# Kernel tuning notes

Measured on AMD Instinct MI355X. Metric: run time of the kernel, lower is better.

The kernel has to match this reference:

```python
import jax, jax.numpy as jnp
import numpy as np


def setup_inputs() -> dict:
    key = jax.random.key(0)
    ks = jax.random.split(key, 6)
    b, l, d, n = 4, 2048, 1024, 16
    scale_d = 1.0 / np.sqrt(d)
    x = jax.random.normal(ks[0], (b, l, d), dtype=jnp.float32)
    W1 = jax.random.normal(ks[1], (d, d), dtype=jnp.float32) * scale_d
    b1 = jnp.zeros((d,), dtype=jnp.float32)
    W2 = jax.random.normal(ks[2], (n, d), dtype=jnp.float32) * scale_d
    b2 = jnp.zeros((n,), dtype=jnp.float32)
    W3 = jax.random.normal(ks[3], (n, d), dtype=jnp.float32) * scale_d
    b3 = jnp.zeros((n,), dtype=jnp.float32)
    A = jax.random.normal(ks[4], (d, n), dtype=jnp.float32) * np.sqrt(2.0 / (d + n))
    return {"x": x, "W1": W1, "b1": b1, "W2": W2, "b2": b2, "W3": W3, "b3": b3, "A": A}


def reference(x, W1, b1, W2, b2, W3, b3, A):
    # delta = softplus(fc1(x)); B = fc2(x); C = fc3(x)
    delta = jax.nn.softplus(jnp.einsum('bld,ed->ble', x, W1) + b1)   # (b,l,d)
    B = jnp.einsum('bld,nd->bln', x, W2) + b2                         # (b,l,n)
    C = jnp.einsum('bld,nd->bln', x, W3) + b3                         # (b,l,n)
    # Discretization: dB = delta \otimes B; dA = exp(delta \otimes A).
    # In the original forward, h is zero-initialized so dA * h == 0 exactly
    # (for both values and gradients); h_new = x[...,None] * dB.
    dB = jnp.einsum('bld,bln->bldn', delta, B)                        # (b,l,d,n)
    h = x[..., None] * dB                                             # (b,l,d,n)
    y = jnp.einsum('bln,bldn->bld', C, h)                             # (b,l,d)
    return y
```

## Files before the change

### kernel.cpp

```cpp
#include <hip/hip_runtime.h>
#include <hip/hip_bf16.h>

typedef __attribute__((ext_vector_type(8))) short bf16x8;
typedef __attribute__((ext_vector_type(8))) unsigned short u16x8;
typedef __attribute__((ext_vector_type(4))) float f32x4;

#define DDIM 1024
#define BM 256
#define BN 128
#define BK 64

__device__ __forceinline__ void gload_lds16(const void* g, void* l) {
  __builtin_amdgcn_global_load_lds((const __attribute__((address_space(1))) void*)g,
                                   (__attribute__((address_space(3))) void*)l,
                                   16, 0, 0);
}

__device__ __forceinline__ unsigned short f2bf(float f) {
  unsigned int u = __float_as_uint(f);
  unsigned int r = (u + 0x7FFFu + ((u >> 16) & 1u)) >> 16;
  return (unsigned short)r;
}

__global__ __launch_bounds__(256) void s6_convert(
    const float* __restrict__ X, const float* __restrict__ W1,
    const float* __restrict__ W2, const float* __restrict__ W3,
    unsigned short* __restrict__ Xbf, unsigned short* __restrict__ W1bf,
    unsigned short* __restrict__ W2bf, unsigned short* __restrict__ W3bf)
{
  const int wid = threadIdx.x >> 6, lane = threadIdx.x & 63;
  const int row = blockIdx.x * 4 + wid;
  const float* src;
  unsigned short* dst;
  if (row < 8192)      { src = X  + (size_t)row * DDIM;        dst = Xbf  + (size_t)row * DDIM; }
  else if (row < 9216) { int r = row - 8192; src = W1 + (size_t)r * DDIM; dst = W1bf + (size_t)r * DDIM; }
  else if (row < 9232) { int r = row - 9216; src = W2 + (size_t)r * DDIM; dst = W2bf + (size_t)r * DDIM; }
  else                 { int r = row - 9232; src = W3 + (size_t)r * DDIM; dst = W3bf + (size_t)r * DDIM; }

  const float4* s4 = reinterpret_cast<const float4*>(src + lane * 16);
  unsigned short u[16];
  #pragma unroll
  for (int j = 0; j < 4; ++j) {
    float4 v = s4[j];
    u[j*4+0] = f2bf(v.x); u[j*4+1] = f2bf(v.y);
    u[j*4+2] = f2bf(v.z); u[j*4+3] = f2bf(v.w);
  }
  u16x8* d8 = reinterpret_cast<u16x8*>(dst + lane * 16);
  u16x8 lo, hi;
  #pragma unroll
  for (int j = 0; j < 8; ++j) { lo[j] = u[j]; hi[j] = u[j + 8]; }
  d8[0] = lo; d8[1] = hi;
}

__global__ __launch_bounds__(512, 2) void s6_main_fused(
    const unsigned short* __restrict__ Xbf,
    const unsigned short* __restrict__ W1bf,
    const unsigned short* __restrict__ W2bf,
    const unsigned short* __restrict__ W3bf,
    const float* __restrict__ b1,
    const float* __restrict__ b2,
    const float* __restrict__ b3,
    float* __restrict__ Y)
{
  __shared__ __align__(16) unsigned short lds[2 * 16384 + 2 * 12288];
  unsigned short* AB = lds;
  unsigned short* BB = lds + 2 * 16384;

  const int tid  = threadIdx.x;
  const int wid  = tid >> 6;
  const int lane = tid & 63;
  const int tile = (blockIdx.x & 7) * 32 + (blockIdx.x >> 3);
  const int rb   = tile >> 3;
  const int cb   = tile & 7;
  const int row0 = rb * BM;
  const int col0 = cb * BN;
  const int wr = wid >> 1, wc = wid & 1;

  const f32x4 z4 = {0.f, 0.f, 0.f, 0.f};
  f32x4 acc[4][4];
  #pragma unroll
  for (int i = 0; i < 4; ++i)
    #pragma unroll
    for (int j = 0; j < 4; ++j)
      acc[i][j] = z4;
  f32x4 accS[4] = {z4, z4, z4, z4};

  const int srow = tid >> 3;
  const int sdch = (lane & 7) ^ (lane >> 3);
  const unsigned short* gaBase = Xbf  + (size_t)(row0 + srow) * DDIM + sdch * 8;
  const unsigned short* gbBase = W1bf + (size_t)(col0 + srow) * DDIM + sdch * 8;
  const int sub = srow;
  const unsigned short* gwsrc;
  if (sub < 16)      gwsrc = W2bf + (size_t)sub * DDIM;
  else if (sub < 32) gwsrc = W3bf + (size_t)(sub - 16) * DDIM;
  else               gwsrc = W2bf + (size_t)(sub & 15) * DDIM;
  const unsigned short* gwBase = gwsrc + sdch * 8;

  const int fr = lane & 15;
  const int swz0 = (((lane >> 4) + 0) ^ (fr & 7)) * 8;
  const int swz1 = (((lane >> 4) + 4) ^ (fr & 7)) * 8;

#define STAGE(BUF, KEL) do {                                                   \
    const unsigned short* sa_ = gaBase + (KEL);                                \
    const unsigned short* sb_ = gbBase + (KEL);                                \
    unsigned short* la_ = AB + (BUF) * 16384 + wid * 512;                      \
    unsigned short* lb_ = BB + (BUF) * 12288 + wid * 512;                      \
    gload_lds16(sa_,                la_);                                      \
    gload_lds16(sa_ +  64 * DDIM,   la_ + 4096);                               \
    gload_lds16(sa_ + 128 * DDIM,   la_ + 8192);                               \
    gload_lds16(sa_ + 192 * DDIM,   la_ + 12288);                              \
    gload_lds16(sb_,                lb_);                                      \
    gload_lds16(sb_ +  64 * DDIM,   lb_ + 4096);                               \
    gload_lds16(gwBase + (KEL),     lb_ + 8192);                               \
  } while (0)

#define COMPUTE(PAR) do {                                                      \
    const unsigned short* Al = AB + (PAR) * 16384;                             \
    const unsigned short* Bl = BB + (PAR) * 12288;                             \
    bf16x8 af[4][2], bfr[4][2], wfr[2];                                        \
    _Pragma("unroll")                                                          \
    for (int m = 0; m < 4; ++m) {                                              \
      af[m][0] = *reinterpret_cast<const bf16x8*>(&Al[(wr*64 + m*16 + fr)*BK + swz0]); \
      af[m][1] = *reinterpret_cast<const bf16x8*>(&Al[(wr*64 + m*16 + fr)*BK + swz1]); \
    }                                                                          \
    _Pragma("unroll")                                                          \
    for (int n = 0; n < 4; ++n) {                                              \
      bfr[n][0] = *reinterpret_cast<const bf16x8*>(&Bl[(wc*64 + n*16 + fr)*BK + swz0]); \
      bfr[n][1] = *reinterpret_cast<const bf16x8*>(&Bl[(wc*64 + n*16 + fr)*BK + swz1]); \
    }                                                                          \
    wfr[0] = *reinterpret_cast<const bf16x8*>(&Bl[(128 + wc*16 + fr)*BK + swz0]); \
    wfr[1] = *reinterpret_cast<const bf16x8*>(&Bl[(128 + wc*16 + fr)*BK + swz1]); \
    __builtin_amdgcn_s_setprio(1);                                             \
    _Pragma("unroll")                                                          \
    for (int ks = 0; ks < 2; ++ks) {                                           \
      _Pragma("unroll")                                                        \
      for (int m = 0; m < 4; ++m) {                                            \
        _Pragma("unroll")                                                      \
        for (int n = 0; n < 4; ++n)                                            \
          acc[m][n] = __builtin_amdgcn_mfma_f32_16x16x32_bf16(af[m][ks], bfr[n][ks], acc[m][n], 0, 0, 0); \
        accS[m] = __builtin_amdgcn_mfma_f32_16x16x32_bf16(af[m][ks], wfr[ks], accS[m], 0, 0, 0); \
      }                                                                        \
    }                                                                          \
    __builtin_amdgcn_s_setprio(0);                                             \
  } while (0)

#define STEP(J, PAR) do {                                                      \
    if ((J) < 15) {                                                            \
      STAGE((PAR) ^ 1, ((J) + 1) * BK);                                        \
      asm volatile("s_waitcnt vmcnt(7)" ::: "memory");                         \
    } else {                                                                   \
      asm volatile("s_waitcnt vmcnt(0)" ::: "memory");                         \
    }                                                                          \
    __builtin_amdgcn_s_barrier();                                              \
    __builtin_amdgcn_sched_barrier(0);                                         \
    COMPUTE(PAR);                                                              \
    __builtin_amdgcn_s_barrier();                                              \
  } while (0)

  STAGE(0, 0);
  asm volatile("s_waitcnt vmcnt(0)" ::: "memory");
  __builtin_amdgcn_s_barrier();

  for (int jj = 0; jj < 16; jj += 2) {
    STEP(jj, 0);
    STEP(jj + 1, 1);
  }
#undef STEP
#undef COMPUTE
#undef STAGE

  float* sEx = (float*)lds;
  const int n_  = lane & 15;
  const int rgp = (lane >> 4) * 4;
  const float bSelf = (wc == 0 ? b2[n_] : b3[n_]);
  #pragma unroll
  for (int m = 0; m < 4; ++m)
    #pragma unroll
    for (int q = 0; q < 4; ++q)
      sEx[(wc * 256 + wr * 64 + m * 16 + rgp + q) * 17 + n_] = accS[m][q] + bSelf;
  __syncthreads();

  float sv[4][4];
  #pragma unroll
  for (int m = 0; m < 4; ++m) {
    #pragma unroll
    for (int q = 0; q < 4; ++q) {
      const float other = sEx[((wc ^ 1) * 256 + wr * 64 + m * 16 + rgp + q) * 17 + n_];
      float p = (accS[m][q] + bSelf) * other;
      p += __shfl_xor(p, 1, 64);
      p += __shfl_xor(p, 2, 64);
      p += __shfl_xor(p, 4, 64);
      p += __shfl_xor(p, 8, 64);
      sv[m][q] = p;
    }
  }

  #pragma unroll
  for (int m = 0; m < 4; ++m) {
    #pragma unroll
    for (int q = 0; q < 4; ++q) {
      const int gr = row0 + wr * 64 + m * 16 + rgp + q;
      const float svv = sv[m][q];
      const size_t rbase = (size_t)gr * DDIM;
      #pragma unroll
      for (int n = 0; n < 4; ++n) {
        const int gc = col0 + wc * 64 + n * 16 + fr;
        const float z  = acc[m][n][q] + b1[gc];
        const float sp = fmaxf(z, 0.f) + __logf(1.f + __expf(-fabsf(z)));
        const float xv = __bfloat162float(*(const __hip_bfloat16*)&Xbf[rbase + gc]);
        Y[rbase + gc] = xv * svv * sp;
      }
    }
  }
}

extern "C" void kernel_launch(void* const* d_in, const int* in_sizes, int n_in,
                              void* d_out, int out_size, void* d_ws, size_t ws_size,
                              hipStream_t stream) {
  const float* x  = (const float*)d_in[0];
  const float* W1 = (const float*)d_in[1];
  const float* b1 = (const float*)d_in[2];
  const float* W2 = (const float*)d_in[3];
  const float* b2 = (const float*)d_in[4];
  const float* W3 = (const float*)d_in[5];
  const float* b3 = (const float*)d_in[6];

  char* ws = (char*)d_ws;
  unsigned short* Xbf  = (unsigned short*)(ws);
  unsigned short* W1bf = (unsigned short*)(ws + 16777216);
  unsigned short* W2bf = (unsigned short*)(ws + 16777216 + 2097152);
  unsigned short* W3bf = (unsigned short*)(ws + 16777216 + 2097152 + 32768);

  s6_convert<<<2312, 256, 0, stream>>>(x, W1, W2, W3, Xbf, W1bf, W2bf, W3bf);
  s6_main_fused<<<256, 512, 0, stream>>>(Xbf, W1bf, W2bf, W3bf, b1, b2, b3,
                                         (float*)d_out);
}
```

Measured before the change: 44.35 us.

## Interleave global-to-LDS staging with MFMA phases in fine-grained K-loop schedule

Restructures the main GEMM loop into four sub-phases per K-tile. Each phase reads a few LDS fragments, issues part of the next tile's global-to-LDS loads, and runs a group of MFMAs, with barriers and priority hints between phases. The goal is to spread memory issue across compute and lower register pressure by loading fewer fragments at a time. The cost is more barriers and lgkmcnt waits per iteration, which could serialize the waves.

```diff
diff --git a/kernel.cpp b/kernel.cpp
--- a/kernel.cpp
+++ b/kernel.cpp
@@ -100,74 +100,119 @@
   const int swz0 = (((lane >> 4) + 0) ^ (fr & 7)) * 8;
   const int swz1 = (((lane >> 4) + 4) ^ (fr & 7)) * 8;
 
-#define STAGE(BUF, KEL) do {                                                   \
-    const unsigned short* sa_ = gaBase + (KEL);                                \
-    const unsigned short* sb_ = gbBase + (KEL);                                \
-    unsigned short* la_ = AB + (BUF) * 16384 + wid * 512;                      \
-    unsigned short* lb_ = BB + (BUF) * 12288 + wid * 512;                      \
-    gload_lds16(sa_,                la_);                                      \
-    gload_lds16(sa_ +  64 * DDIM,   la_ + 4096);                               \
-    gload_lds16(sa_ + 128 * DDIM,   la_ + 8192);                               \
-    gload_lds16(sa_ + 192 * DDIM,   la_ + 12288);                              \
-    gload_lds16(sb_,                lb_);                                      \
-    gload_lds16(sb_ +  64 * DDIM,   lb_ + 4096);                               \
-    gload_lds16(gwBase + (KEL),     lb_ + 8192);                               \
-  } while (0)
-
-#define COMPUTE(PAR) do {                                                      \
-    const unsigned short* Al = AB + (PAR) * 16384;                             \
-    const unsigned short* Bl = BB + (PAR) * 12288;                             \
-    bf16x8 af[4][2], bfr[4][2], wfr[2];                                        \
-    _Pragma("unroll")                                                          \
-    for (int m = 0; m < 4; ++m) {                                              \
-      af[m][0] = *reinterpret_cast<const bf16x8*>(&Al[(wr*64 + m*16 + fr)*BK + swz0]); \
-      af[m][1] = *reinterpret_cast<const bf16x8*>(&Al[(wr*64 + m*16 + fr)*BK + swz1]); \
-    }                                                                          \
-    _Pragma("unroll")                                                          \
-    for (int n = 0; n < 4; ++n) {                                              \
-      bfr[n][0] = *reinterpret_cast<const bf16x8*>(&Bl[(wc*64 + n*16 + fr)*BK + swz0]); \
-      bfr[n][1] = *reinterpret_cast<const bf16x8*>(&Bl[(wc*64 + n*16 + fr)*BK + swz1]); \
-    }                                                                          \
-    wfr[0] = *reinterpret_cast<const bf16x8*>(&Bl[(128 + wc*16 + fr)*BK + swz0]); \
-    wfr[1] = *reinterpret_cast<const bf16x8*>(&Bl[(128 + wc*16 + fr)*BK + swz1]); \
-    __builtin_amdgcn_s_setprio(1);                                             \
-    _Pragma("unroll")                                                          \
-    for (int ks = 0; ks < 2; ++ks) {                                           \
-      _Pragma("unroll")                                                        \
-      for (int m = 0; m < 4; ++m) {                                            \
-        _Pragma("unroll")                                                      \
-        for (int n = 0; n < 4; ++n)                                            \
-          acc[m][n] = __builtin_amdgcn_mfma_f32_16x16x32_bf16(af[m][ks], bfr[n][ks], acc[m][n], 0, 0, 0); \
-        accS[m] = __builtin_amdgcn_mfma_f32_16x16x32_bf16(af[m][ks], wfr[ks], accS[m], 0, 0, 0); \
-      }                                                                        \
-    }                                                                          \
-    __builtin_amdgcn_s_setprio(0);                                             \
-  } while (0)
-
-#define STEP(J, PAR) do {                                                      \
-    if ((J) < 15) {                                                            \
-      STAGE((PAR) ^ 1, ((J) + 1) * BK);                                        \
-      asm volatile("s_waitcnt vmcnt(7)" ::: "memory");                         \
-    } else {                                                                   \
-      asm volatile("s_waitcnt vmcnt(0)" ::: "memory");                         \
-    }                                                                          \
-    __builtin_amdgcn_s_barrier();                                              \
-    __builtin_amdgcn_sched_barrier(0);                                         \
-    COMPUTE(PAR);                                                              \
-    __builtin_amdgcn_s_barrier();                                              \
-  } while (0)
-
-  STAGE(0, 0);
+#define SA(BUF, KEL, SEG) gload_lds16(gaBase + (KEL) + (SEG) * 64 * DDIM,      \
+                                      AB + (BUF) * 16384 + wid * 512 + (SEG) * 4096)
+#define SB(BUF, KEL, SEG) gload_lds16(gbBase + (KEL) + (SEG) * 64 * DDIM,      \
+                                      BB + (BUF) * 12288 + wid * 512 + (SEG) * 4096)
+#define SW(BUF, KEL)      gload_lds16(gwBase + (KEL),                          \
+                                      BB + (BUF) * 12288 + wid * 512 + 8192)
+#define RA(M, SWZ) (*reinterpret_cast<const bf16x8*>(&Al[(wr * 64 + (M) * 16 + fr) * BK + (SWZ)]))
+#define RB(N, SWZ) (*reinterpret_cast<const bf16x8*>(&Bl[(wc * 64 + (N) * 16 + fr) * BK + (SWZ)]))
+#define RW(SWZ)    (*reinterpret_cast<const bf16x8*>(&Bl[(128 + wc * 16 + fr) * BK + (SWZ)]))
+#define BAR()   __builtin_amdgcn_s_barrier()
+#define SCB()   __builtin_amdgcn_sched_barrier(0)
+#define LGKM0() asm volatile("s_waitcnt lgkmcnt(0)" ::: "memory")
+
+  SA(0, 0, 0); SA(0, 0, 1); SA(0, 0, 2); SA(0, 0, 3);
+  SB(0, 0, 0); SB(0, 0, 1); SW(0, 0);
   asm volatile("s_waitcnt vmcnt(0)" ::: "memory");
-  __builtin_amdgcn_s_barrier();
-
-  for (int jj = 0; jj < 16; jj += 2) {
-    STEP(jj, 0);
-    STEP(jj + 1, 1);
-  }
-#undef STEP
-#undef COMPUTE
-#undef STAGE
+  BAR(); SCB();
+
+  for (int t = 0; t < 16; ++t) {
+    const int par = t & 1;
+    const int nb  = par ^ 1;
+    const int kn  = (t + 1) * BK;
+    const unsigned short* Al = AB + par * 16384;
+    const unsigned short* Bl = BB + par * 12288;
+    bf16x8 a0, a1, a2, a3, f0, f1, f2, f3, wf;
+
+    if (t < 15) {
+      SA(nb, kn, 0); SA(nb, kn, 1);
+      asm volatile("s_waitcnt vmcnt(2)" ::: "memory");
+    } else {
+      asm volatile("s_waitcnt vmcnt(0)" ::: "memory");
+    }
+    BAR(); SCB();
+    a0 = RA(0, swz0); a1 = RA(1, swz0);
+    f0 = RB(0, swz0); f1 = RB(1, swz0); f2 = RB(2, swz0); f3 = RB(3, swz0);
+    wf = RW(swz0);
+    LGKM0(); SCB();
+    __builtin_amdgcn_s_setprio(1);
+    acc[0][0] = __builtin_amdgcn_mfma_f32_16x16x32_bf16(a0, f0, acc[0][0], 0, 0, 0);
+    acc[0][1] = __builtin_amdgcn_mfma_f32_16x16x32_bf16(a0, f1, acc[0][1], 0, 0, 0);
+    acc[0][2] = __builtin_amdgcn_mfma_f32_16x16x32_bf16(a0, f2, acc[0][2], 0, 0, 0);
+    acc[0][3] = __builtin_amdgcn_mfma_f32_16x16x32_bf16(a0, f3, acc[0][3], 0, 0, 0);
+    acc[1][0] = __builtin_amdgcn_mfma_f32_16x16x32_bf16(a1, f0, acc[1][0], 0, 0, 0);
+    acc[1][1] = __builtin_amdgcn_mfma_f32_16x16x32_bf16(a1, f1, acc[1][1], 0, 0, 0);
+    acc[1][2] = __builtin_amdgcn_mfma_f32_16x16x32_bf16(a1, f2, acc[1][2], 0, 0, 0);
+    acc[1][3] = __builtin_amdgcn_mfma_f32_16x16x32_bf16(a1, f3, acc[1][3], 0, 0, 0);
+    __builtin_amdgcn_s_setprio(0);
+    BAR(); SCB();
+
+    a2 = RA(2, swz0); a3 = RA(3, swz0);
+    if (t < 15) { SA(nb, kn, 2); SA(nb, kn, 3); }
+    BAR(); SCB();
+    LGKM0(); SCB();
+    __builtin_amdgcn_s_setprio(1);
+    acc[2][0] = __builtin_amdgcn_mfma_f32_16x16x32_bf16(a2, f0, acc[2][0], 0, 0, 0);
+    acc[2][1] = __builtin_amdgcn_mfma_f32_16x16x32_bf16(a2, f1, acc[2][1], 0, 0, 0);
+    acc[2][2] = __builtin_amdgcn_mfma_f32_16x16x32_bf16(a2, f2, acc[2][2], 0, 0, 0);
+    acc[2][3] = __builtin_amdgcn_mfma_f32_16x16x32_bf16(a2, f3, acc[2][3], 0, 0, 0);
+    acc[3][0] = __builtin_amdgcn_mfma_f32_16x16x32_bf16(a3, f0, acc[3][0], 0, 0, 0);
+    acc[3][1] = __builtin_amdgcn_mfma_f32_16x16x32_bf16(a3, f1, acc[3][1], 0, 0, 0);
+    acc[3][2] = __builtin_amdgcn_mfma_f32_16x16x32_bf16(a3, f2, acc[3][2], 0, 0, 0);
+    acc[3][3] = __builtin_amdgcn_mfma_f32_16x16x32_bf16(a3, f3, acc[3][3], 0, 0, 0);
+    accS[0]   = __builtin_amdgcn_mfma_f32_16x16x32_bf16(a0, wf, accS[0], 0, 0, 0);
+    accS[1]   = __builtin_amdgcn_mfma_f32_16x16x32_bf16(a1, wf, accS[1], 0, 0, 0);
+    accS[2]   = __builtin_amdgcn_mfma_f32_16x16x32_bf16(a2, wf, accS[2], 0, 0, 0);
+    accS[3]   = __builtin_amdgcn_mfma_f32_16x16x32_bf16(a3, wf, accS[3], 0, 0, 0);
+    __builtin_amdgcn_s_setprio(0);
+    BAR(); SCB();
+
+    a0 = RA(0, swz1); a1 = RA(1, swz1);
+    f0 = RB(0, swz1); f1 = RB(1, swz1); f2 = RB(2, swz1); f3 = RB(3, swz1);
+    wf = RW(swz1);
+    if (t < 15) { SB(nb, kn, 0); SB(nb, kn, 1); }
+    BAR(); SCB();
+    LGKM0(); SCB();
+    __builtin_amdgcn_s_setprio(1);
+    acc[0][0] = __builtin_amdgcn_mfma_f32_16x16x32_bf16(a0, f0, acc[0][0], 0, 0, 0);
+    acc[0][1] = __builtin_amdgcn_mfma_f32_16x16x32_bf16(a0, f1, acc[0][1], 0, 0, 0);
+    acc[0][2] = __builtin_amdgcn_mfma_f32_16x16x32_bf16(a0, f2, acc[0][2], 0, 0, 0);
+    acc[0][3] = __builtin_amdgcn_mfma_f32_16x16x32_bf16(a0, f3, acc[0][3], 0, 0, 0);
+    acc[1][0] = __builtin_amdgcn_mfma_f32_16x16x32_bf16(a1, f0, acc[1][0], 0, 0, 0);
+    acc[1][1] = __builtin_amdgcn_mfma_f32_16x16x32_bf16(a1, f1, acc[1][1], 0, 0, 0);
+    acc[1][2] = __builtin_amdgcn_mfma_f32_16x16x32_bf16(a1, f2, acc[1][2], 0, 0, 0);
+    acc[1][3] = __builtin_amdgcn_mfma_f32_16x16x32_bf16(a1, f3, acc[1][3], 0, 0, 0);
+    __builtin_amdgcn_s_setprio(0);
+    BAR(); SCB();
+
+    a2 = RA(2, swz1); a3 = RA(3, swz1);
+    if (t < 15) { SW(nb, kn); }
+    BAR(); SCB();
+    LGKM0(); SCB();
+    __builtin_amdgcn_s_setprio(1);
+    acc[2][0] = __builtin_amdgcn_mfma_f32_16x16x32_bf16(a2, f0, acc[2][0], 0, 0, 0);
+    acc[2][1] = __builtin_amdgcn_mfma_f32_16x16x32_bf16(a2, f1, acc[2][1], 0, 0, 0);
+    acc[2][2] = __builtin_amdgcn_mfma_f32_16x16x32_bf16(a2, f2, acc[2][2], 0, 0, 0);
+    acc[2][3] = __builtin_amdgcn_mfma_f32_16x16x32_bf16(a2, f3, acc[2][3], 0, 0, 0);
+    acc[3][0] = __builtin_amdgcn_mfma_f32_16x16x32_bf16(a3, f0, acc[3][0], 0, 0, 0);
+    acc[3][1] = __builtin_amdgcn_mfma_f32_16x16x32_bf16(a3, f1, acc[3][1], 0, 0, 0);
+    acc[3][2] = __builtin_amdgcn_mfma_f32_16x16x32_bf16(a3, f2, acc[3][2], 0, 0, 0);
+    acc[3][3] = __builtin_amdgcn_mfma_f32_16x16x32_bf16(a3, f3, acc[3][3], 0, 0, 0);
+    accS[0]   = __builtin_amdgcn_mfma_f32_16x16x32_bf16(a0, wf, accS[0], 0, 0, 0);
+    accS[1]   = __builtin_amdgcn_mfma_f32_16x16x32_bf16(a1, wf, accS[1], 0, 0, 0);
+    accS[2]   = __builtin_amdgcn_mfma_f32_16x16x32_bf16(a2, wf, accS[2], 0, 0, 0);
+    accS[3]   = __builtin_amdgcn_mfma_f32_16x16x32_bf16(a3, wf, accS[3], 0, 0, 0);
+    __builtin_amdgcn_s_setprio(0);
+    BAR(); SCB();
+  }
+#undef SA
+#undef SB
+#undef SW
+#undef RA
+#undef RB
+#undef RW
 
   float* sEx = (float*)lds;
   const int n_  = lane & 15;
```

Result: no change. 44.65 us (+0.7%).

## Fuse x fp32-to-bf16 conversion into GEMM A-tile loading

Applied to the files above, without the earlier changes.

The separate pre-pass that converted x to bf16 is removed. The main kernel now loads fp32 x rows into registers, converts them to bf16 and writes the swizzled A tile to LDS itself, while W tiles still use direct global-to-LDS loads. This saves writing and re-reading a 16 MB bf16 copy and shrinks the convert kernel to weights only. In exchange it doubles global read bytes for the A tile per k-step, which every column block re-reads, and adds register pressure and VALU conversion work inside the pipelined loop. The epilogue now reads x directly in fp32.

```diff
diff --git a/kernel.cpp b/kernel.cpp
--- a/kernel.cpp
+++ b/kernel.cpp
@@ -22,20 +22,19 @@
   return (unsigned short)r;
 }
 
-__global__ __launch_bounds__(256) void s6_convert(
-    const float* __restrict__ X, const float* __restrict__ W1,
-    const float* __restrict__ W2, const float* __restrict__ W3,
-    unsigned short* __restrict__ Xbf, unsigned short* __restrict__ W1bf,
-    unsigned short* __restrict__ W2bf, unsigned short* __restrict__ W3bf)
+__global__ __launch_bounds__(256) void s6_convert_w(
+    const float* __restrict__ W1, const float* __restrict__ W2,
+    const float* __restrict__ W3,
+    unsigned short* __restrict__ W1bf, unsigned short* __restrict__ W2bf,
+    unsigned short* __restrict__ W3bf)
 {
   const int wid = threadIdx.x >> 6, lane = threadIdx.x & 63;
   const int row = blockIdx.x * 4 + wid;
   const float* src;
   unsigned short* dst;
-  if (row < 8192)      { src = X  + (size_t)row * DDIM;        dst = Xbf  + (size_t)row * DDIM; }
-  else if (row < 9216) { int r = row - 8192; src = W1 + (size_t)r * DDIM; dst = W1bf + (size_t)r * DDIM; }
-  else if (row < 9232) { int r = row - 9216; src = W2 + (size_t)r * DDIM; dst = W2bf + (size_t)r * DDIM; }
-  else                 { int r = row - 9232; src = W3 + (size_t)r * DDIM; dst = W3bf + (size_t)r * DDIM; }
+  if (row < 1024)      { src = W1 + (size_t)row * DDIM;          dst = W1bf + (size_t)row * DDIM; }
+  else if (row < 1040) { int r = row - 1024; src = W2 + (size_t)r * DDIM; dst = W2bf + (size_t)r * DDIM; }
+  else                 { int r = row - 1040; src = W3 + (size_t)r * DDIM; dst = W3bf + (size_t)r * DDIM; }
 
   const float4* s4 = reinterpret_cast<const float4*>(src + lane * 16);
   unsigned short u[16];
@@ -53,7 +52,7 @@
 }
 
 __global__ __launch_bounds__(512, 2) void s6_main_fused(
-    const unsigned short* __restrict__ Xbf,
+    const float* __restrict__ X,
     const unsigned short* __restrict__ W1bf,
     const unsigned short* __restrict__ W2bf,
     const unsigned short* __restrict__ W3bf,
@@ -85,9 +84,13 @@
       acc[i][j] = z4;
   f32x4 accS[4] = {z4, z4, z4, z4};
 
+  const int arow  = tid >> 1;
+  const int ahalf = tid & 1;
+  const int arow7 = arow & 7;
+  const float* gA = X + (size_t)(row0 + arow) * DDIM + ahalf * 32;
+
   const int srow = tid >> 3;
   const int sdch = (lane & 7) ^ (lane >> 3);
-  const unsigned short* gaBase = Xbf  + (size_t)(row0 + srow) * DDIM + sdch * 8;
   const unsigned short* gbBase = W1bf + (size_t)(col0 + srow) * DDIM + sdch * 8;
   const int sub = srow;
   const unsigned short* gwsrc;
@@ -100,19 +103,30 @@
   const int swz0 = (((lane >> 4) + 0) ^ (fr & 7)) * 8;
   const int swz1 = (((lane >> 4) + 4) ^ (fr & 7)) * 8;
 
-#define STAGE(BUF, KEL) do {                                                   \
-    const unsigned short* sa_ = gaBase + (KEL);                                \
-    const unsigned short* sb_ = gbBase + (KEL);                                \
-    unsigned short* la_ = AB + (BUF) * 16384 + wid * 512;                      \
-    unsigned short* lb_ = BB + (BUF) * 12288 + wid * 512;                      \
-    gload_lds16(sa_,                la_);                                      \
-    gload_lds16(sa_ +  64 * DDIM,   la_ + 4096);                               \
-    gload_lds16(sa_ + 128 * DDIM,   la_ + 8192);                               \
-    gload_lds16(sa_ + 192 * DDIM,   la_ + 12288);                              \
-    gload_lds16(sb_,                lb_);                                      \
-    gload_lds16(sb_ +  64 * DDIM,   lb_ + 4096);                               \
-    gload_lds16(gwBase + (KEL),     lb_ + 8192);                               \
+  float4 av[8];
+
+#define ALOAD(KEL) do {                                                        \
+    const float* g_ = gA + (KEL);                                              \
+    _Pragma("unroll")                                                          \
+    for (int j = 0; j < 8; ++j) av[j] = *reinterpret_cast<const float4*>(g_ + j * 4); \
   } while (0)
+
+#define AWRITE(BUF) do {                                                       \
+    unsigned short* base_ = AB + (BUF) * 16384 + arow * 64;                    \
+    _Pragma("unroll")                                                          \
+    for (int c = 0; c < 4; ++c) {                                              \
+      u16x8 w_;                                                                \
+      float4 lo_ = av[c * 2], hi_ = av[c * 2 + 1];                             \
+      w_[0] = f2bf(lo_.x); w_[1] = f2bf(lo_.y); w_[2] = f2bf(lo_.z); w_[3] = f2bf(lo_.w); \
+      w_[4] = f2bf(hi_.x); w_[5] = f2bf(hi_.y); w_[6] = f2bf(hi_.z); w_[7] = f2bf(hi_.w); \
+      *reinterpret_cast<u16x8*>(base_ + (((ahalf * 4 + c) ^ arow7) * 8)) = w_; \
+    }                                                                          \
+  } while (0)
+
+#define SB(BUF, KEL, SEG) gload_lds16(gbBase + (KEL) + (SEG) * 64 * DDIM,      \
+                                      BB + (BUF) * 12288 + wid * 512 + (SEG) * 4096)
+#define SW(BUF, KEL)      gload_lds16(gwBase + (KEL),                          \
+                                      BB + (BUF) * 12288 + wid * 512 + 8192)
 
 #define COMPUTE(PAR) do {                                                      \
     const unsigned short* Al = AB + (PAR) * 16384;                             \
@@ -144,30 +158,29 @@
     __builtin_amdgcn_s_setprio(0);                                             \
   } while (0)
 
-#define STEP(J, PAR) do {                                                      \
-    if ((J) < 15) {                                                            \
-      STAGE((PAR) ^ 1, ((J) + 1) * BK);                                        \
-      asm volatile("s_waitcnt vmcnt(7)" ::: "memory");                         \
-    } else {                                                                   \
-      asm volatile("s_waitcnt vmcnt(0)" ::: "memory");                         \
-    }                                                                          \
-    __builtin_amdgcn_s_barrier();                                              \
-    __builtin_amdgcn_sched_barrier(0);                                         \
-    COMPUTE(PAR);                                                              \
-    __builtin_amdgcn_s_barrier();                                              \
-  } while (0)
-
-  STAGE(0, 0);
-  asm volatile("s_waitcnt vmcnt(0)" ::: "memory");
-  __builtin_amdgcn_s_barrier();
-
-  for (int jj = 0; jj < 16; jj += 2) {
-    STEP(jj, 0);
-    STEP(jj + 1, 1);
-  }
-#undef STEP
+  ALOAD(0);
+  SB(0, 0, 0); SB(0, 0, 1); SW(0, 0);
+  AWRITE(0);
+  __syncthreads();
+
+  for (int t = 0; t < 16; ++t) {
+    const int cur = t & 1;
+    const int nb  = cur ^ 1;
+    const int kn  = (t + 1) * BK;
+    if (t < 15) {
+      ALOAD(kn);
+      SB(nb, kn, 0); SB(nb, kn, 1); SW(nb, kn);
+    }
+    __builtin_amdgcn_sched_barrier(0);
+    COMPUTE(cur);
+    if (t < 15) AWRITE(nb);
+    __syncthreads();
+  }
+#undef ALOAD
+#undef AWRITE
+#undef SB
+#undef SW
 #undef COMPUTE
-#undef STAGE
 
   float* sEx = (float*)lds;
   const int n_  = lane & 15;
@@ -207,7 +220,7 @@
         const int gc = col0 + wc * 64 + n * 16 + fr;
         const float z  = acc[m][n][q] + b1[gc];
         const float sp = fmaxf(z, 0.f) + __logf(1.f + __expf(-fabsf(z)));
-        const float xv = __bfloat162float(*(const __hip_bfloat16*)&Xbf[rbase + gc]);
+        const float xv = X[rbase + gc];
         Y[rbase + gc] = xv * svv * sp;
       }
     }
@@ -226,12 +239,11 @@
   const float* b3 = (const float*)d_in[6];
 
   char* ws = (char*)d_ws;
-  unsigned short* Xbf  = (unsigned short*)(ws);
-  unsigned short* W1bf = (unsigned short*)(ws + 16777216);
-  unsigned short* W2bf = (unsigned short*)(ws + 16777216 + 2097152);
-  unsigned short* W3bf = (unsigned short*)(ws + 16777216 + 2097152 + 32768);
-
-  s6_convert<<<2312, 256, 0, stream>>>(x, W1, W2, W3, Xbf, W1bf, W2bf, W3bf);
-  s6_main_fused<<<256, 512, 0, stream>>>(Xbf, W1bf, W2bf, W3bf, b1, b2, b3,
+  unsigned short* W1bf = (unsigned short*)(ws);
+  unsigned short* W2bf = (unsigned short*)(ws + 2097152);
+  unsigned short* W3bf = (unsigned short*)(ws + 2097152 + 32768);
+
+  s6_convert_w<<<264, 256, 0, stream>>>(W1, W2, W3, W1bf, W2bf, W3bf);
+  s6_main_fused<<<256, 512, 0, stream>>>(x, W1bf, W2bf, W3bf, b1, b2, b3,
                                          (float*)d_out);
 }
```

Result: slower. 72.83 us (+64.2%).
